# Optimization experiments

Measured on AMD Instinct MI355X. Metric: run time of the kernel, lower is better.

The kernel has to match this reference:

```python
import jax, jax.numpy as jnp
import numpy as np

D_MODEL = 1024
D_INNER = 1024
N_HEADS = 16
HEAD_DIM = D_INNER // N_HEADS  # 64
D_STATE = 16
DT_RANK = 16
CHUNK = 64
PROJ = 2 * D_INNER + 2 * D_STATE * N_HEADS + DT_RANK  # 2576


def setup_inputs() -> dict:
    key = jax.random.key(0)
    ks = jax.random.split(key, 6)
    B, S = 4, 4096
    x = jax.random.normal(ks[0], (B, S, D_MODEL), jnp.float32)
    W_in = jax.random.normal(ks[1], (PROJ, D_MODEL), jnp.float32) * 0.02
    dt_W = jax.random.normal(ks[2], (N_HEADS, DT_RANK), jnp.float32) * 0.1
    dt_b = jax.random.normal(ks[3], (N_HEADS,), jnp.float32) * 0.1
    A_log = jnp.full((N_HEADS,), jnp.log(0.5), jnp.float32)
    D_param = jnp.ones((N_HEADS,), jnp.float32)
    W_out = jax.random.normal(ks[4], (D_MODEL, D_INNER), jnp.float32) * 0.02
    norm_w = jnp.ones((D_INNER,), jnp.float32)
    return dict(x=x, W_in=W_in, dt_W=dt_W, dt_b=dt_b, A_log=A_log,
                D_param=D_param, W_out=W_out, norm_w=norm_w)


def _forward(x, W_in, dt_W, dt_b, A_log, D_param, W_out, norm_w):
    B, S, _ = x.shape
    H, P, N, K = N_HEADS, HEAD_DIM, D_STATE, CHUNK
    proj = x @ W_in.T  # (B,S,PROJ)
    xp = proj[..., :D_INNER]
    z = proj[..., D_INNER:2 * D_INNER]
    o = 2 * D_INNER
    B_ssm = proj[..., o:o + N * H].reshape(B, S, H, N)
    C_ssm = proj[..., o + N * H:o + 2 * N * H].reshape(B, S, H, N)
    dt_low = proj[..., o + 2 * N * H:]
    dt = jax.nn.softplus(dt_low @ dt_W.T + dt_b)  # (B,S,H)
    xp = xp.reshape(B, S, H, P)
    A = -jnp.exp(A_log)  # (H,)

    # --- chunked selective scan (SSD) ---
    nC = S // K  # S chosen divisible by K (original pads otherwise)
    xc = xp.reshape(B, nC, K, H, P)
    dtc = dt.reshape(B, nC, K, H)
    Bc = B_ssm.reshape(B, nC, K, H, N)
    Cc = C_ssm.reshape(B, nC, K, H, N)
    dA = dtc * A  # (B,nC,K,H)
    dAcs = jnp.cumsum(dA, axis=2)
    # intra-chunk quadratic (attention-like) form
    Lm = jnp.exp(dAcs[:, :, :, None, :] - dAcs[:, :, None, :, :])
    causal = jnp.tril(jnp.ones((K, K), jnp.float32))
    Lm = Lm * causal[None, None, :, :, None]
    scores = jnp.einsum('bcihn,bcjhn->bcijh', Cc, Bc) * Lm * dtc[:, :, None, :, :]
    y_intra = jnp.einsum('bcijh,bcjhp->bcihp', scores, xc)
    # per-chunk state contribution
    decay_to_end = jnp.exp(dAcs[:, :, -1:, :] - dAcs)
    wx = (dtc * decay_to_end)[..., None] * xc  # (B,nC,K,H,P)
    chunk_state = jnp.einsum('bckhn,bckhp->bchnp', Bc, wx)  # (B,nC,H,N,P)
    chunk_decay = jnp.exp(dAcs[:, :, -1, :])  # (B,nC,H)

    # cross-chunk recurrence: emit state at chunk START (matches torch loop)
    def step(h, inp):
        d, s = inp
        return d[:, :, None, None] * h + s, h
    h0 = jnp.zeros((B, H, N, P), jnp.float32)
    _, h_states = jax.lax.scan(
        step, h0,
        (jnp.moveaxis(chunk_decay, 1, 0), jnp.moveaxis(chunk_state, 1, 0)))
    h_states = jnp.moveaxis(h_states, 0, 1)  # (B,nC,H,N,P)

    y_cross = jnp.einsum('bcthn,bchnp,bcth->bcthp', Cc, h_states, jnp.exp(dAcs))
    y = (y_intra + y_cross).reshape(B, S, H, P)
    # --- end scan ---

    y = y + xp * D_param[None, None, :, None]
    y = y.reshape(B, S, D_INNER)
    rms = jnp.sqrt(jnp.mean(y * y, axis=-1, keepdims=True) + 1e-6)
    y = y / rms * norm_w
    y = y * jax.nn.silu(z)
    return y @ W_out.T


def reference(x, W_in, dt_W, dt_b, A_log, D_param, W_out, norm_w):
    return _forward(x, W_in, dt_W, dt_b, A_log, D_param, W_out, norm_w)
```

## Files before the change

### kernel.cpp

```cpp
#include <hip/hip_runtime.h>

typedef unsigned short u16;
typedef __attribute__((ext_vector_type(8))) short short8;
typedef __attribute__((ext_vector_type(4))) float f32x4;
typedef __attribute__((ext_vector_type(4))) unsigned short u16x4;
typedef __attribute__((ext_vector_type(8))) unsigned short u16x8;

#define BTOK 16384
#define PROJ_N 2576
#define PROJ_PAD 2688
#define DK 1024
#define NCH 256
#define NH 16
#define HD 64
#define NS 16

__device__ __forceinline__ float b2f(u16 b) {
    union { unsigned int u; float f; } v; v.u = ((unsigned int)b) << 16; return v.f;
}
__device__ __forceinline__ u16 f2b(float f) {
    union { float f; unsigned int u; } v; v.f = f;
    unsigned int r = v.u + 0x7fffu + ((v.u >> 16) & 1u);
    return (u16)(r >> 16);
}
__device__ __forceinline__ void gl_lds16(const u16* g, u16* l) {
    __builtin_amdgcn_global_load_lds((__attribute__((address_space(1))) void*)g,
                                     (__attribute__((address_space(3))) void*)l,
                                     16, 0, 0);
}

__global__ __launch_bounds__(256) void cast_bf16(const float* __restrict__ s,
                                                 u16* __restrict__ d, int n4) {
    int t = blockIdx.x * 256 + threadIdx.x;
    if (t < n4) {
        float4 v = ((const float4*)s)[t];
        u16x4 o; o.x = f2b(v.x); o.y = f2b(v.y); o.z = f2b(v.z); o.w = f2b(v.w);
        ((u16x4*)d)[t] = o;
    }
}

__global__ __launch_bounds__(256) void cast_pad_win(const float* __restrict__ s,
                                                    u16* __restrict__ d) {
    int t = blockIdx.x * 256 + threadIdx.x;
    int i4 = t * 4;
    float4 v = make_float4(0.f, 0.f, 0.f, 0.f);
    if (i4 < PROJ_N * DK) v = ((const float4*)s)[t];
    u16x4 o; o.x = f2b(v.x); o.y = f2b(v.y); o.z = f2b(v.z); o.w = f2b(v.w);
    ((u16x4*)d)[t] = o;
}

template <int OUT_BF16>
__global__ __launch_bounds__(256) void gemm_bt(const u16* __restrict__ A,
                                               const u16* __restrict__ B,
                                               float* __restrict__ Cf,
                                               u16* __restrict__ Cb,
                                               int K, int ldc) {
    __shared__ u16 As[128 * 64];
    __shared__ u16 Bs[128 * 64];
    const int tid = threadIdx.x;
    const int bm = blockIdx.x, bn = blockIdx.y;
    const int wave = tid >> 6, lane = tid & 63;
    const int wm = (wave >> 1) * 64, wn = (wave & 1) * 64;
    const int m_l = lane & 15, quad = lane >> 4;

    f32x4 acc[4][4];
#pragma unroll
    for (int i = 0; i < 4; ++i)
#pragma unroll
        for (int j = 0; j < 4; ++j) acc[i][j] = (f32x4){0.f, 0.f, 0.f, 0.f};

    const u16* Ab = A + (long)bm * 128 * K;
    const u16* Bb = B + (long)bn * 128 * K;

    for (int k0 = 0; k0 < K; k0 += 64) {
#pragma unroll
        for (int it = 0; it < 4; ++it) {
            int li = it * 256 + tid;
            int r = li >> 3;
            int k8 = (li & 7) ^ (r & 7);
            u16* lbase = &As[(it * 256 + wave * 64) * 8];
            gl_lds16(Ab + (long)r * K + k0 + k8 * 8, lbase);
            u16* lbaseB = &Bs[(it * 256 + wave * 64) * 8];
            gl_lds16(Bb + (long)r * K + k0 + k8 * 8, lbaseB);
        }
        __syncthreads();
#pragma unroll
        for (int ks = 0; ks < 2; ++ks) {
            const int k8 = ks * 4 + quad;
            const int slot = k8 ^ (m_l & 7);
            short8 af[4], bf[4];
#pragma unroll
            for (int i = 0; i < 4; ++i) af[i] = *(const short8*)(&As[(wm + i * 16 + m_l) * 64 + slot * 8]);
#pragma unroll
            for (int j = 0; j < 4; ++j) bf[j] = *(const short8*)(&Bs[(wn + j * 16 + m_l) * 64 + slot * 8]);
#pragma unroll
            for (int i = 0; i < 4; ++i)
#pragma unroll
                for (int j = 0; j < 4; ++j)
                    acc[i][j] = __builtin_amdgcn_mfma_f32_16x16x32_bf16(af[i], bf[j], acc[i][j], 0, 0, 0);
        }
        __syncthreads();
    }
#pragma unroll
    for (int i = 0; i < 4; ++i) {
        int row_base = bm * 128 + wm + i * 16 + quad * 4;
#pragma unroll
        for (int j = 0; j < 4; ++j) {
            int col = bn * 128 + wn + j * 16 + m_l;
#pragma unroll
            for (int r = 0; r < 4; ++r) {
                float v = acc[i][j][r];
                long off = (long)(row_base + r) * ldc + col;
                if (OUT_BF16) Cb[off] = f2b(v);
                else          Cf[off] = v;
            }
        }
    }
}

__global__ __launch_bounds__(256) void ssm_intra(const u16* __restrict__ proj,
                                                 const float* __restrict__ dt_W,
                                                 const float* __restrict__ dt_b,
                                                 const float* __restrict__ A_log,
                                                 float* __restrict__ dAcs,
                                                 float* __restrict__ decay,
                                                 u16* __restrict__ y_acc,
                                                 float* __restrict__ cstate) {
    int bch = blockIdx.x;
    int bc = bch >> 4, h = bch & 15;
    long tok0 = (long)bc * 64;
    __shared__ float Cs[64][20], Bm[64][20];
    __shared__ u16 Sh[64][72], Sl[64][72];
    __shared__ u16 Xt[64][72];
    __shared__ u16 Wh[64][72], Wl[64][72];
    __shared__ u16 Bt[16][72];
    __shared__ float dts[64], dAs[64], wk[64];
    const int tid = threadIdx.x;
    const int wave = tid >> 6, lane = tid & 63;
    const int m_l = lane & 15, quad = lane >> 4;

    if (tid < 64) {
        long tok = tok0 + tid;
        u16x8 lo0 = *(const u16x8*)&proj[tok * PROJ_PAD + 2560];
        u16x8 lo1 = *(const u16x8*)&proj[tok * PROJ_PAD + 2568];
        float a = dt_b[h];
#pragma unroll
        for (int r = 0; r < 8; ++r) a += b2f(lo0[r]) * dt_W[h * 16 + r];
#pragma unroll
        for (int r = 0; r < 8; ++r) a += b2f(lo1[r]) * dt_W[h * 16 + 8 + r];
        float d = (a > 20.f) ? a : log1pf(__expf(a));
        float dA = -__expf(A_log[h]) * d;
        float cs = dA;
#pragma unroll
        for (int off = 1; off < 64; off <<= 1) {
            float o = __shfl_up(cs, off, 64);
            if (tid >= off) cs += o;
        }
        float cs63 = __shfl(cs, 63, 64);
        dts[tid] = d;
        dAs[tid] = cs;
        wk[tid] = d * __expf(cs63 - cs);
        dAcs[tok * 16 + h] = cs;
        if (tid == 63) decay[bc * 16 + h] = __expf(cs);
    }
#pragma unroll
    for (int it = 0; it < 4; ++it) {
        int li = it * 256 + tid;
        int i = li >> 4, n = li & 15;
        u16 cb = proj[(tok0 + i) * PROJ_PAD + 2304 + h * 16 + n];
        u16 bb = proj[(tok0 + i) * PROJ_PAD + 2048 + h * 16 + n];
        Cs[i][n] = b2f(cb);
        Bm[i][n] = b2f(bb);
        Bt[n][i] = bb;
    }
    __syncthreads();
#pragma unroll
    for (int it = 0; it < 2; ++it) {
        int li = it * 256 + tid;
        int j = li & 63, p0 = (li >> 6) * 8;
        u16x8 xv = *(const u16x8*)&proj[(tok0 + j) * PROJ_PAD + h * 64 + p0];
        float w = wk[j];
#pragma unroll
        for (int t = 0; t < 8; ++t) {
            u16 xb = xv[t];
            Xt[p0 + t][j] = xb;
            float v = w * b2f(xb);
            u16 hi = f2b(v);
            Wh[p0 + t][j] = hi;
            Wl[p0 + t][j] = f2b(v - b2f(hi));
        }
    }
    {
        int j = tid & 63, i0 = tid >> 6;
#pragma unroll
        for (int g = 0; g < 16; ++g) {
            int i = i0 + g * 4;
            float v = 0.f;
            if (j <= i) {
                float d = 0.f;
                const f32x4* cp = (const f32x4*)Cs[i];
                const f32x4* bp = (const f32x4*)Bm[j];
#pragma unroll
                for (int n4 = 0; n4 < 4; ++n4) {
                    f32x4 c = cp[n4], b = bp[n4];
                    d += c.x * b.x + c.y * b.y + c.z * b.z + c.w * b.w;
                }
                v = d * __expf(dAs[i] - dAs[j]) * dts[j];
            }
            u16 hi = f2b(v);
            Sh[i][j] = hi;
            Sl[i][j] = f2b(v - b2f(hi));
        }
    }
    __syncthreads();
    {
        f32x4 yv[4];
#pragma unroll
        for (int jt = 0; jt < 4; ++jt) yv[jt] = (f32x4){0.f, 0.f, 0.f, 0.f};
#pragma unroll
        for (int ks = 0; ks < 2; ++ks) {
            int kc = ks * 32 + quad * 8;
            short8 ah = *(const short8*)&Sh[wave * 16 + m_l][kc];
            short8 al = *(const short8*)&Sl[wave * 16 + m_l][kc];
#pragma unroll
            for (int jt = 0; jt < 4; ++jt) {
                short8 bx = *(const short8*)&Xt[jt * 16 + m_l][kc];
                yv[jt] = __builtin_amdgcn_mfma_f32_16x16x32_bf16(ah, bx, yv[jt], 0, 0, 0);
                yv[jt] = __builtin_amdgcn_mfma_f32_16x16x32_bf16(al, bx, yv[jt], 0, 0, 0);
            }
        }
#pragma unroll
        for (int jt = 0; jt < 4; ++jt)
#pragma unroll
            for (int r = 0; r < 4; ++r) {
                int i = wave * 16 + quad * 4 + r;
                int p = jt * 16 + m_l;
                y_acc[(tok0 + i) * 1024 + h * 64 + p] = f2b(yv[jt][r]);
            }
    }
    {
        f32x4 cacc = (f32x4){0.f, 0.f, 0.f, 0.f};
#pragma unroll
        for (int ks = 0; ks < 2; ++ks) {
            int kc = ks * 32 + quad * 8;
            short8 a = *(const short8*)&Bt[m_l][kc];
            short8 bh = *(const short8*)&Wh[wave * 16 + m_l][kc];
            short8 bl = *(const short8*)&Wl[wave * 16 + m_l][kc];
            cacc = __builtin_amdgcn_mfma_f32_16x16x32_bf16(a, bh, cacc, 0, 0, 0);
            cacc = __builtin_amdgcn_mfma_f32_16x16x32_bf16(a, bl, cacc, 0, 0, 0);
        }
#pragma unroll
        for (int r = 0; r < 4; ++r) {
            int n = quad * 4 + r;
            int p = wave * 16 + m_l;
            cstate[(long)bch * 1024 + n * 64 + p] = cacc[r];
        }
    }
}

__global__ __launch_bounds__(256) void scan_chunks(const float* __restrict__ cs,
                                                   const float* __restrict__ decay,
                                                   float* __restrict__ hs) {
    int t = blockIdx.x * 256 + threadIdx.x;
    int p = t & 63, n = (t >> 6) & 15, h = (t >> 10) & 15, b = t >> 14;
    float state = 0.f;
    for (int c = 0; c < 64; ++c) {
        long idx = (((long)((b * 64 + c) * 16 + h)) * 16 + n) * 64 + p;
        hs[idx] = state;
        state = decay[(b * 64 + c) * 16 + h] * state + cs[idx];
    }
}

__global__ __launch_bounds__(256) void ssm_cross(const u16* __restrict__ proj,
                                                 const float* __restrict__ dAcs,
                                                 const float* __restrict__ hs,
                                                 const u16* __restrict__ y_acc,
                                                 const float* __restrict__ D_param,
                                                 u16* __restrict__ y_pre) {
    int bch = blockIdx.x;
    int bc = bch >> 4, h = bch & 15;
    long tok0 = (long)bc * 64;
    __shared__ float hss[16][64], Cs[64][16], dAs[64];
    int tid = threadIdx.x;
#pragma unroll
    for (int it = 0; it < 4; ++it) {
        int li = it * 256 + tid;
        hss[li >> 6][li & 63] = hs[(long)bch * 1024 + li];
        int i = li >> 4, n = li & 15;
        Cs[i][n] = b2f(proj[(tok0 + i) * PROJ_PAD + 2304 + h * 16 + n]);
    }
    if (tid < 64) dAs[tid] = dAcs[(tok0 + tid) * 16 + h];
    __syncthreads();
    float Dh = D_param[h];
    int pi = (tid & 15) * 4;
    int ib = tid >> 4;
#pragma unroll
    for (int g = 0; g < 4; ++g) {
        int i = ib + 16 * g;
        f32x4 cr = (f32x4){0.f, 0.f, 0.f, 0.f};
#pragma unroll
        for (int n = 0; n < 16; ++n) {
            float c = Cs[i][n];
            cr += c * *(const f32x4*)&hss[n][pi];
        }
        float e = __expf(dAs[i]);
        long off = (tok0 + i) * 1024 + h * 64 + pi;
        u16x4 ya = *(const u16x4*)&y_acc[off];
        u16x4 xv = *(const u16x4*)&proj[(tok0 + i) * PROJ_PAD + h * 64 + pi];
        u16x4 o;
        o.x = f2b(b2f(ya.x) + e * cr.x + b2f(xv.x) * Dh);
        o.y = f2b(b2f(ya.y) + e * cr.y + b2f(xv.y) * Dh);
        o.z = f2b(b2f(ya.z) + e * cr.z + b2f(xv.z) * Dh);
        o.w = f2b(b2f(ya.w) + e * cr.w + b2f(xv.w) * Dh);
        *(u16x4*)&y_pre[off] = o;
    }
}

__global__ __launch_bounds__(256) void norm_gate(const u16* __restrict__ proj,
                                                 const float* __restrict__ norm_w,
                                                 u16* __restrict__ y) {
    long tok = blockIdx.x;
    int tid = threadIdx.x;
    int c0 = tid * 4;
    u16x4 yv = *(const u16x4*)&y[tok * 1024 + c0];
    float v0 = b2f(yv.x), v1 = b2f(yv.y), v2 = b2f(yv.z), v3 = b2f(yv.w);
    float ss = v0 * v0 + v1 * v1 + v2 * v2 + v3 * v3;
    int lane = tid & 63, w = tid >> 6;
#pragma unroll
    for (int d = 32; d > 0; d >>= 1) ss += __shfl_down(ss, d, 64);
    __shared__ float red[4];
    if (lane == 0) red[w] = ss;
    __syncthreads();
    float tot = red[0] + red[1] + red[2] + red[3];
    float inv = rsqrtf(tot * (1.f / 1024.f) + 1e-6f);
    float4 nw = *(const float4*)&norm_w[c0];
    u16x4 zv = *(const u16x4*)&proj[tok * PROJ_PAD + 1024 + c0];
    float z0 = b2f(zv.x), z1 = b2f(zv.y), z2 = b2f(zv.z), z3 = b2f(zv.w);
    u16x4 o;
    o.x = f2b(v0 * inv * nw.x * (z0 / (1.f + __expf(-z0))));
    o.y = f2b(v1 * inv * nw.y * (z1 / (1.f + __expf(-z1))));
    o.z = f2b(v2 * inv * nw.z * (z2 / (1.f + __expf(-z2))));
    o.w = f2b(v3 * inv * nw.w * (z3 / (1.f + __expf(-z3))));
    *(u16x4*)&y[tok * 1024 + c0] = o;
}

extern "C" void kernel_launch(void* const* d_in, const int* in_sizes, int n_in,
                              void* d_out, int out_size, void* d_ws, size_t ws_size,
                              hipStream_t stream) {
    const float* x      = (const float*)d_in[0];
    const float* W_in   = (const float*)d_in[1];
    const float* dt_W   = (const float*)d_in[2];
    const float* dt_b   = (const float*)d_in[3];
    const float* A_log  = (const float*)d_in[4];
    const float* D_par  = (const float*)d_in[5];
    const float* W_out  = (const float*)d_in[6];
    const float* norm_w = (const float*)d_in[7];
    float* out = (float*)d_out;

    char* ws = (char*)d_ws;
    size_t off = 0;
    auto alloc = [&](size_t b) { void* p = ws + off; off += (b + 255) & ~(size_t)255; return p; };
    u16*   x_bf    = (u16*)alloc((size_t)BTOK * DK * 2);
    u16*   win_bf  = (u16*)alloc((size_t)PROJ_PAD * DK * 2);
    u16*   wout_bf = (u16*)alloc((size_t)DK * DK * 2);
    u16*   proj    = (u16*)alloc((size_t)BTOK * PROJ_PAD * 2);
    float* dAcs    = (float*)alloc((size_t)BTOK * NH * 4);
    float* decay   = (float*)alloc((size_t)NCH * NH * 4);
    float* cstate  = (float*)alloc((size_t)NCH * NH * NS * HD * 4);
    float* hstates = (float*)alloc((size_t)NCH * NH * NS * HD * 4);
    u16*   y_pre   = (u16*)alloc((size_t)BTOK * DK * 2);
    u16*   y_acc   = x_bf;

    cast_bf16<<<BTOK * DK / 4 / 256, 256, 0, stream>>>(x, x_bf, BTOK * DK / 4);
    cast_bf16<<<DK * DK / 4 / 256, 256, 0, stream>>>(W_out, wout_bf, DK * DK / 4);
    cast_pad_win<<<PROJ_PAD * DK / 4 / 256, 256, 0, stream>>>(W_in, win_bf);

    gemm_bt<1><<<dim3(128, 21), 256, 0, stream>>>(x_bf, win_bf, nullptr, proj, DK, PROJ_PAD);

    ssm_intra<<<NCH * NH, 256, 0, stream>>>(proj, dt_W, dt_b, A_log, dAcs, decay, y_acc, cstate);
    scan_chunks<<<256, 256, 0, stream>>>(cstate, decay, hstates);
    ssm_cross<<<NCH * NH, 256, 0, stream>>>(proj, dAcs, hstates, y_acc, D_par, y_pre);
    norm_gate<<<BTOK, 256, 0, stream>>>(proj, norm_w, y_pre);

    gemm_bt<0><<<dim3(128, 8), 256, 0, stream>>>(y_pre, wout_bf, out, nullptr, DK, DK);
}
```

Measured before the change: 393.5 us.

## Replace GEMM with 256x256-tile, 8-wave, double-buffered pipelined kernel

Both projection GEMMs now use a 512-thread kernel with 256x256 output tiles in 128 KB of dynamic LDS. Global-to-LDS loads are double-buffered and interleaved with MFMA phases using explicit vmcnt waits, raised wave priority around the MFMA blocks, and an XCD-aware remap of block IDs. The aim is more data reuse per tile and hiding load latency behind compute. The cost is padding PROJ_PAD to 2816 (extra wasted columns) and fewer, larger blocks, which can leave the GPU underfilled on the small output GEMM.

Result: no change. 400.0 us (+1.6%).

```diff
diff --git a/kernel.cpp b/kernel.cpp
--- a/kernel.cpp
+++ b/kernel.cpp
@@ -8,7 +8,7 @@
 
 #define BTOK 16384
 #define PROJ_N 2576
-#define PROJ_PAD 2688
+#define PROJ_PAD 2816
 #define DK 1024
 #define NCH 256
 #define NH 16
@@ -28,6 +28,9 @@
                                      (__attribute__((address_space(3))) void*)l,
                                      16, 0, 0);
 }
+
+#define BAR() do { asm volatile("" ::: "memory"); __builtin_amdgcn_s_barrier(); asm volatile("" ::: "memory"); } while (0)
+#define MFMA_B16 __builtin_amdgcn_mfma_f32_16x16x32_bf16
 
 __global__ __launch_bounds__(256) void cast_bf16(const float* __restrict__ s,
                                                  u16* __restrict__ d, int n4) {
@@ -49,67 +52,157 @@
     ((u16x4*)d)[t] = o;
 }
 
+#define MT 64
+
 template <int OUT_BF16>
-__global__ __launch_bounds__(256) void gemm_bt(const u16* __restrict__ A,
-                                               const u16* __restrict__ B,
-                                               float* __restrict__ Cf,
-                                               u16* __restrict__ Cb,
-                                               int K, int ldc) {
-    __shared__ u16 As[128 * 64];
-    __shared__ u16 Bs[128 * 64];
+__global__ __launch_bounds__(512, 2) void gemm8(const u16* __restrict__ A,
+                                                const u16* __restrict__ B,
+                                                float* __restrict__ Cf,
+                                                u16* __restrict__ Cb,
+                                                int K, int ldc) {
+    extern __shared__ u16 smem[];
+    u16* AsU = smem;
+    u16* BsU = smem + 32768;
     const int tid = threadIdx.x;
-    const int bm = blockIdx.x, bn = blockIdx.y;
     const int wave = tid >> 6, lane = tid & 63;
-    const int wm = (wave >> 1) * 64, wn = (wave & 1) * 64;
+    const int wr = wave >> 2, wc = wave & 3;
     const int m_l = lane & 15, quad = lane >> 4;
 
-    f32x4 acc[4][4];
-#pragma unroll
-    for (int i = 0; i < 4; ++i)
-#pragma unroll
-        for (int j = 0; j < 4; ++j) acc[i][j] = (f32x4){0.f, 0.f, 0.f, 0.f};
-
-    const u16* Ab = A + (long)bm * 128 * K;
-    const u16* Bb = B + (long)bn * 128 * K;
-
-    for (int k0 = 0; k0 < K; k0 += 64) {
-#pragma unroll
-        for (int it = 0; it < 4; ++it) {
-            int li = it * 256 + tid;
-            int r = li >> 3;
-            int k8 = (li & 7) ^ (r & 7);
-            u16* lbase = &As[(it * 256 + wave * 64) * 8];
-            gl_lds16(Ab + (long)r * K + k0 + k8 * 8, lbase);
-            u16* lbaseB = &Bs[(it * 256 + wave * 64) * 8];
-            gl_lds16(Bb + (long)r * K + k0 + k8 * 8, lbaseB);
-        }
-        __syncthreads();
-#pragma unroll
-        for (int ks = 0; ks < 2; ++ks) {
-            const int k8 = ks * 4 + quad;
-            const int slot = k8 ^ (m_l & 7);
-            short8 af[4], bf[4];
-#pragma unroll
-            for (int i = 0; i < 4; ++i) af[i] = *(const short8*)(&As[(wm + i * 16 + m_l) * 64 + slot * 8]);
-#pragma unroll
-            for (int j = 0; j < 4; ++j) bf[j] = *(const short8*)(&Bs[(wn + j * 16 + m_l) * 64 + slot * 8]);
-#pragma unroll
-            for (int i = 0; i < 4; ++i)
-#pragma unroll
-                for (int j = 0; j < 4; ++j)
-                    acc[i][j] = __builtin_amdgcn_mfma_f32_16x16x32_bf16(af[i], bf[j], acc[i][j], 0, 0, 0);
-        }
-        __syncthreads();
-    }
-#pragma unroll
-    for (int i = 0; i < 4; ++i) {
-        int row_base = bm * 128 + wm + i * 16 + quad * 4;
-#pragma unroll
-        for (int j = 0; j < 4; ++j) {
-            int col = bn * 128 + wn + j * 16 + m_l;
+    int id = blockIdx.x;
+    const int cpx = gridDim.x >> 3;
+    id = (id & 7) * cpx + (id >> 3);
+    const int bm = id & (MT - 1);
+    const int bn = id >> 6;
+
+    const u16* Ab = A + (long)bm * 256 * K;
+    const u16* Bb = B + (long)bn * 256 * K;
+
+    const int sw = m_l & 7;
+    const int aoff0 = (wr * 128 + m_l) * 64 + (quad ^ sw) * 8;
+    const int aoff1 = (wr * 128 + m_l) * 64 + ((4 + quad) ^ sw) * 8;
+    const int boff0 = (wc * 64 + m_l) * 64 + (quad ^ sw) * 8;
+    const int boff1 = (wc * 64 + m_l) * 64 + ((4 + quad) ^ sw) * 8;
+
+    const int srow = tid >> 3;
+    const int schk = (tid & 7) ^ (srow & 7);
+    const int sdst = wave * 512;
+
+    f32x4 acc[8][4];
+#pragma unroll
+    for (int f = 0; f < 8; ++f)
+#pragma unroll
+        for (int n = 0; n < 4; ++n) acc[f][n] = (f32x4){0.f, 0.f, 0.f, 0.f};
+
+    const int NT = K >> 6;
+
+    auto stage = [&](const u16* G, u16* L, int q, int k0) {
+        gl_lds16(G + (long)(q * 64 + srow) * K + k0 + schk * 8,
+                 L + q * 4096 + sdst);
+    };
+
+    stage(Ab, AsU, 0, 0); stage(Ab, AsU, 2, 0);
+    stage(Bb, BsU, 0, 0); stage(Bb, BsU, 1, 0); stage(Bb, BsU, 2, 0); stage(Bb, BsU, 3, 0);
+    stage(Ab, AsU, 1, 0); stage(Ab, AsU, 3, 0);
+    stage(Ab, AsU + 16384, 0, 64); stage(Ab, AsU + 16384, 2, 64);
+    asm volatile("s_waitcnt vmcnt(2)" ::: "memory");
+    BAR();
+
+    short8 af[4][2], bf[4][2];
+    int cur = 0;
+    for (int t = 0; t < NT; ++t) {
+        const int cb = cur << 14;
+        const int nb = cb ^ 16384;
+        u16* Acur = AsU + cb; u16* Anxt = AsU + nb;
+        u16* Bnxt = BsU + nb; const u16* Bcur = BsU + cb;
+        const int k1 = (t + 1) << 6, k2 = (t + 2) << 6;
+        const bool s1 = (t + 1 < NT), s2 = (t + 2 < NT);
+
+#pragma unroll
+        for (int f = 0; f < 4; ++f) {
+            af[f][0] = *(const short8*)(Acur + aoff0 + f * 1024);
+            af[f][1] = *(const short8*)(Acur + aoff1 + f * 1024);
+        }
+#pragma unroll
+        for (int n = 0; n < 2; ++n) {
+            bf[n][0] = *(const short8*)(Bcur + boff0 + n * 1024);
+            bf[n][1] = *(const short8*)(Bcur + boff1 + n * 1024);
+        }
+        if (s1) { stage(Bb, Bnxt, 0, k1); stage(Bb, Bnxt, 1, k1);
+                  stage(Bb, Bnxt, 2, k1); stage(Bb, Bnxt, 3, k1); }
+        BAR();
+        __builtin_amdgcn_s_setprio(1);
+#pragma unroll
+        for (int f = 0; f < 4; ++f)
+#pragma unroll
+            for (int n = 0; n < 2; ++n) {
+                acc[f][n] = MFMA_B16(af[f][0], bf[n][0], acc[f][n], 0, 0, 0);
+                acc[f][n] = MFMA_B16(af[f][1], bf[n][1], acc[f][n], 0, 0, 0);
+            }
+        __builtin_amdgcn_s_setprio(0);
+        BAR();
+
+#pragma unroll
+        for (int n = 0; n < 2; ++n) {
+            bf[2 + n][0] = *(const short8*)(Bcur + boff0 + (2 + n) * 1024);
+            bf[2 + n][1] = *(const short8*)(Bcur + boff1 + (2 + n) * 1024);
+        }
+        if (s1) { stage(Ab, Anxt, 1, k1); stage(Ab, Anxt, 3, k1); }
+        BAR();
+        __builtin_amdgcn_s_setprio(1);
+#pragma unroll
+        for (int f = 0; f < 4; ++f)
+#pragma unroll
+            for (int n = 0; n < 2; ++n) {
+                acc[f][2 + n] = MFMA_B16(af[f][0], bf[2 + n][0], acc[f][2 + n], 0, 0, 0);
+                acc[f][2 + n] = MFMA_B16(af[f][1], bf[2 + n][1], acc[f][2 + n], 0, 0, 0);
+            }
+        __builtin_amdgcn_s_setprio(0);
+        if (s1) { asm volatile("s_waitcnt vmcnt(8)" ::: "memory"); }
+        else    { asm volatile("s_waitcnt vmcnt(0)" ::: "memory"); }
+        BAR();
+
+#pragma unroll
+        for (int f = 0; f < 4; ++f) {
+            af[f][0] = *(const short8*)(Acur + aoff0 + 4096 + f * 1024);
+            af[f][1] = *(const short8*)(Acur + aoff1 + 4096 + f * 1024);
+        }
+        if (s2) { stage(Ab, Acur, 0, k2); stage(Ab, Acur, 2, k2); }
+        BAR();
+        __builtin_amdgcn_s_setprio(1);
+#pragma unroll
+        for (int f = 0; f < 4; ++f)
+#pragma unroll
+            for (int n = 0; n < 2; ++n) {
+                acc[4 + f][n] = MFMA_B16(af[f][0], bf[n][0], acc[4 + f][n], 0, 0, 0);
+                acc[4 + f][n] = MFMA_B16(af[f][1], bf[n][1], acc[4 + f][n], 0, 0, 0);
+            }
+        __builtin_amdgcn_s_setprio(0);
+        BAR();
+
+        __builtin_amdgcn_s_setprio(1);
+#pragma unroll
+        for (int f = 0; f < 4; ++f)
+#pragma unroll
+            for (int n = 0; n < 2; ++n) {
+                acc[4 + f][2 + n] = MFMA_B16(af[f][0], bf[2 + n][0], acc[4 + f][2 + n], 0, 0, 0);
+                acc[4 + f][2 + n] = MFMA_B16(af[f][1], bf[2 + n][1], acc[4 + f][2 + n], 0, 0, 0);
+            }
+        __builtin_amdgcn_s_setprio(0);
+        if (s1 && s2)      { asm volatile("s_waitcnt vmcnt(4)" ::: "memory"); }
+        else if (s1)       { asm volatile("s_waitcnt vmcnt(2)" ::: "memory"); }
+        BAR();
+        cur ^= 1;
+    }
+
+#pragma unroll
+    for (int f = 0; f < 8; ++f) {
+        int row_base = bm * 256 + wr * 128 + f * 16 + quad * 4;
+#pragma unroll
+        for (int n = 0; n < 4; ++n) {
+            int col = bn * 256 + wc * 64 + n * 16 + m_l;
 #pragma unroll
             for (int r = 0; r < 4; ++r) {
-                float v = acc[i][j][r];
+                float v = acc[f][n][r];
                 long off = (long)(row_base + r) * ldc + col;
                 if (OUT_BF16) Cb[off] = f2b(v);
                 else          Cf[off] = v;
@@ -225,8 +318,8 @@
 #pragma unroll
             for (int jt = 0; jt < 4; ++jt) {
                 short8 bx = *(const short8*)&Xt[jt * 16 + m_l][kc];
-                yv[jt] = __builtin_amdgcn_mfma_f32_16x16x32_bf16(ah, bx, yv[jt], 0, 0, 0);
-                yv[jt] = __builtin_amdgcn_mfma_f32_16x16x32_bf16(al, bx, yv[jt], 0, 0, 0);
+                yv[jt] = MFMA_B16(ah, bx, yv[jt], 0, 0, 0);
+                yv[jt] = MFMA_B16(al, bx, yv[jt], 0, 0, 0);
             }
         }
 #pragma unroll
@@ -246,8 +339,8 @@
             short8 a = *(const short8*)&Bt[m_l][kc];
             short8 bh = *(const short8*)&Wh[wave * 16 + m_l][kc];
             short8 bl = *(const short8*)&Wl[wave * 16 + m_l][kc];
-            cacc = __builtin_amdgcn_mfma_f32_16x16x32_bf16(a, bh, cacc, 0, 0, 0);
-            cacc = __builtin_amdgcn_mfma_f32_16x16x32_bf16(a, bl, cacc, 0, 0, 0);
+            cacc = MFMA_B16(a, bh, cacc, 0, 0, 0);
+            cacc = MFMA_B16(a, bl, cacc, 0, 0, 0);
         }
 #pragma unroll
         for (int r = 0; r < 4; ++r) {
@@ -371,16 +464,25 @@
     u16*   y_pre   = (u16*)alloc((size_t)BTOK * DK * 2);
     u16*   y_acc   = x_bf;
 
+    static bool attr_done = false;
+    if (!attr_done) {
+        hipFuncSetAttribute(reinterpret_cast<const void*>(&gemm8<1>),
+                            hipFuncAttributeMaxDynamicSharedMemorySize, 131072);
+        hipFuncSetAttribute(reinterpret_cast<const void*>(&gemm8<0>),
+                            hipFuncAttributeMaxDynamicSharedMemorySize, 131072);
+        attr_done = true;
+    }
+
     cast_bf16<<<BTOK * DK / 4 / 256, 256, 0, stream>>>(x, x_bf, BTOK * DK / 4);
     cast_bf16<<<DK * DK / 4 / 256, 256, 0, stream>>>(W_out, wout_bf, DK * DK / 4);
     cast_pad_win<<<PROJ_PAD * DK / 4 / 256, 256, 0, stream>>>(W_in, win_bf);
 
-    gemm_bt<1><<<dim3(128, 21), 256, 0, stream>>>(x_bf, win_bf, nullptr, proj, DK, PROJ_PAD);
+    gemm8<1><<<dim3(MT * (PROJ_PAD / 256)), 512, 131072, stream>>>(x_bf, win_bf, nullptr, proj, DK, PROJ_PAD);
 
     ssm_intra<<<NCH * NH, 256, 0, stream>>>(proj, dt_W, dt_b, A_log, dAcs, decay, y_acc, cstate);
     scan_chunks<<<256, 256, 0, stream>>>(cstate, decay, hstates);
     ssm_cross<<<NCH * NH, 256, 0, stream>>>(proj, dAcs, hstates, y_acc, D_par, y_pre);
     norm_gate<<<BTOK, 256, 0, stream>>>(proj, norm_w, y_pre);
 
-    gemm_bt<0><<<dim3(128, 8), 256, 0, stream>>>(y_pre, wout_bf, out, nullptr, DK, DK);
-}
+    gemm8<0><<<dim3(MT * (DK / 256)), 512, 131072, stream>>>(y_pre, wout_bf, out, nullptr, DK, DK);
+}
```
